# Kernel optimization log

Measured on AMD Instinct MI355X. Metric: run time of the kernel, lower is better.

Reference implementation:

```python
import jax, jax.numpy as jnp
import numpy as np

B, S, V, D, H, DK, DH, L = 1, 2048, 256, 1024, 16, 64, 4096, 4
EPS = 1e-5
SCALE = 1.0 / np.sqrt(DK)


def _ln(x, g, b):
    mu = jnp.mean(x, axis=-1, keepdims=True)
    var = jnp.mean(jnp.square(x - mu), axis=-1, keepdims=True)
    return (x - mu) * jax.lax.rsqrt(var + EPS) * g + b


def setup_inputs() -> dict:
    key = jax.random.key(0)
    ks = jax.random.split(key, 20)
    f = lambda k, shape: (0.02 * jax.random.normal(k, shape)).astype(jnp.float32)
    return {
        "x": jax.random.randint(ks[0], (B, S), 0, V),
        "emb": f(ks[1], (V, D)),
        "pos": f(ks[2], (S, D)),
        "Wq": f(ks[3], (L, D, H * DK)), "bq": jnp.zeros((L, H * DK), jnp.float32),
        "Wk": f(ks[4], (L, D, H * DK)), "bk": jnp.zeros((L, H * DK), jnp.float32),
        "Wv": f(ks[5], (L, D, H * DK)), "bv": jnp.zeros((L, H * DK), jnp.float32),
        "Wo": f(ks[6], (L, H * DK, D)),
        "ln1_g": jnp.ones((L, D), jnp.float32), "ln1_b": jnp.zeros((L, D), jnp.float32),
        "W1": f(ks[7], (L, D, DH)), "b1": jnp.zeros((L, DH), jnp.float32),
        "W2": f(ks[8], (L, DH, D)), "b2": jnp.zeros((L, D), jnp.float32),
        "ln2_g": jnp.ones((L, D), jnp.float32), "ln2_b": jnp.zeros((L, D), jnp.float32),
        "head_w": f(ks[9], (D, V)), "head_b": jnp.zeros((V,), jnp.float32),
    }


def _forward(x, emb, pos, Wq, bq, Wk, bk, Wv, bv, Wo, ln1_g, ln1_b,
             W1, b1, W2, b2, ln2_g, ln2_b, head_w, head_b):
    h = emb[x] + pos[:S]                      # [B,S,D]
    causal = jnp.tril(jnp.ones((S, S), bool))  # additive -inf above diag
    for i in range(L):
        # --- naive attention: explicit QK^T, mask, softmax, @V ---
        q = (h @ Wq[i] + bq[i]).reshape(B, S, H, DK)
        k = (h @ Wk[i] + bk[i]).reshape(B, S, H, DK)
        v = (h @ Wv[i] + bv[i]).reshape(B, S, H, DK)
        scores = jnp.einsum('bqhd,bkhd->bhqk', q * SCALE, k)   # [B,H,S,S]
        scores = jnp.where(causal[None, None], scores, -jnp.inf)
        p = jax.nn.softmax(scores, axis=-1)
        a = jnp.einsum('bhqk,bkhd->bqhd', p, v).reshape(B, S, H * DK) @ Wo[i]
        # --- TransformerLayer: x + ln2(mlp(x + ln1(attn(x)))) ---
        u = h + _ln(a, ln1_g[i], ln1_b[i])
        m = jax.nn.gelu(u @ W1[i] + b1[i], approximate=False) @ W2[i] + b2[i]
        h = h + _ln(m, ln2_g[i], ln2_b[i])
    return h @ head_w + head_b                 # [B,S,V]


def reference(x, emb, pos, Wq, bq, Wk, bk, Wv, bv, Wo, ln1_g, ln1_b,
              W1, b1, W2, b2, ln2_g, ln2_b, head_w, head_b):
    return _forward(x, emb, pos, Wq, bq, Wk, bk, Wv, bv, Wo, ln1_g, ln1_b,
                    W1, b1, W2, b2, ln2_g, ln2_b, head_w, head_b)
```

## Files before the change

kernel.cpp:

```cpp
#include <hip/hip_runtime.h>
#include <hip/hip_bf16.h>
#include <cstdint>
#include <math.h>

static constexpr int S_  = 2048;
static constexpr int D_  = 1024;
static constexpr int H_  = 16;
static constexpr int DK_ = 64;
static constexpr int DH_ = 4096;
static constexpr int L_  = 4;
static constexpr int V_  = 256;
#define ATT_SCALE 0.125f

typedef __bf16 bf16;
typedef __bf16 bf16x8 __attribute__((ext_vector_type(8)));
typedef __bf16 bf16x4v __attribute__((ext_vector_type(4)));
typedef float  f32x4  __attribute__((ext_vector_type(4)));

__device__ __forceinline__ __attribute__((address_space(3))) void* to_lds(const void* p) {
  return (__attribute__((address_space(3))) void*)(uintptr_t)p;
}
__device__ __forceinline__ __attribute__((address_space(1))) void* to_glb(const void* p) {
  return (__attribute__((address_space(1))) void*)(uintptr_t)p;
}

template <int GELU_EPI>
__global__ __launch_bounds__(256) void gemm_bf16_kernel(
    const bf16* __restrict__ A, const bf16* __restrict__ Bt,
    const float* __restrict__ bias, float* __restrict__ Cf, bf16* __restrict__ Cb,
    int M, int N, int K)
{
  __shared__ __align__(16) bf16 sA[2][128 * 64];
  __shared__ __align__(16) bf16 sB[2][64 * 64];
  const int tid  = threadIdx.x;
  const int wave = tid >> 6;
  const int lane = tid & 63;
  const int l16  = lane & 15;
  const int quad = lane >> 4;
  const int bm = blockIdx.x * 128;
  const int bn = blockIdx.y * 64;
  const int wm = (wave & 1) * 64;
  const int wn = (wave >> 1) * 32;

  const int srow = tid >> 3;
  const int sc8  = (tid & 7) ^ (srow & 7);
  const bf16* gA = A  + (size_t)(bm + srow) * K + sc8 * 8;
  const bf16* gB = Bt + (size_t)(bn + srow) * K + sc8 * 8;

  const int swz = l16 & 7;

  f32x4 acc[4][2] = {};

#pragma unroll
  for (int u = 0; u < 4; ++u)
    __builtin_amdgcn_global_load_lds(to_glb(gA + (size_t)u * 32 * K),
                                     to_lds(&sA[0][u * 2048 + tid * 8]), 16, 0, 0);
#pragma unroll
  for (int u = 0; u < 2; ++u)
    __builtin_amdgcn_global_load_lds(to_glb(gB + (size_t)u * 32 * K),
                                     to_lds(&sB[0][u * 2048 + tid * 8]), 16, 0, 0);

  int cur = 0;
  for (int k0 = 0; k0 < K; k0 += 64, cur ^= 1) {
    if (k0 + 64 < K) {
      const int nb = cur ^ 1;
      const size_t ko = k0 + 64;
#pragma unroll
      for (int u = 0; u < 4; ++u)
        __builtin_amdgcn_global_load_lds(to_glb(gA + ko + (size_t)u * 32 * K),
                                         to_lds(&sA[nb][u * 2048 + tid * 8]), 16, 0, 0);
#pragma unroll
      for (int u = 0; u < 2; ++u)
        __builtin_amdgcn_global_load_lds(to_glb(gB + ko + (size_t)u * 32 * K),
                                         to_lds(&sB[nb][u * 2048 + tid * 8]), 16, 0, 0);
      asm volatile("s_waitcnt vmcnt(6)" ::: "memory");
    } else {
      asm volatile("s_waitcnt vmcnt(0)" ::: "memory");
    }
    __builtin_amdgcn_s_barrier();

    bf16x8 af[2][4], bfv[2][2];
#pragma unroll
    for (int kc = 0; kc < 2; ++kc) {
      const int c8 = ((kc * 4 + quad) ^ swz) * 8;
#pragma unroll
      for (int i = 0; i < 4; ++i)
        af[kc][i] = *(const bf16x8*)&sA[cur][(wm + i * 16 + l16) * 64 + c8];
#pragma unroll
      for (int j = 0; j < 2; ++j)
        bfv[kc][j] = *(const bf16x8*)&sB[cur][(wn + j * 16 + l16) * 64 + c8];
    }
    asm volatile("s_waitcnt lgkmcnt(0)" ::: "memory");
    __builtin_amdgcn_s_barrier();

#pragma unroll
    for (int kc = 0; kc < 2; ++kc)
#pragma unroll
      for (int i = 0; i < 4; ++i)
#pragma unroll
        for (int j = 0; j < 2; ++j)
          acc[i][j] = __builtin_amdgcn_mfma_f32_16x16x32_bf16(af[kc][i], bfv[kc][j], acc[i][j], 0, 0, 0);
  }

#pragma unroll
  for (int i = 0; i < 4; ++i) {
#pragma unroll
    for (int j = 0; j < 2; ++j) {
      const int col = bn + wn + j * 16 + l16;
      const float bz = bias ? bias[col] : 0.0f;
#pragma unroll
      for (int r = 0; r < 4; ++r) {
        const int row = bm + wm + i * 16 + quad * 4 + r;
        float v = acc[i][j][r] + bz;
        if (GELU_EPI) v = 0.5f * v * (1.0f + erff(v * 0.70710678118654752f));
        if (Cf) Cf[(size_t)row * N + col] = v;
        if (Cb) Cb[(size_t)row * N + col] = (bf16)v;
      }
    }
  }
}

__global__ __launch_bounds__(256) void transpose_cast_kernel(
    const float* __restrict__ in, bf16* __restrict__ out, int K, int N)
{
  __shared__ float t[32][33];
  const int k0 = blockIdx.y * 32;
  const int n0 = blockIdx.x * 32;
  const int tx = threadIdx.x & 31;
  const int ty = threadIdx.x >> 5;
#pragma unroll
  for (int i = 0; i < 32; i += 8)
    t[ty + i][tx] = in[(size_t)(k0 + ty + i) * N + (n0 + tx)];
  __syncthreads();
#pragma unroll
  for (int i = 0; i < 32; i += 8)
    out[(size_t)(n0 + ty + i) * K + (k0 + tx)] = (bf16)t[tx][ty + i];
}

__global__ __launch_bounds__(256) void transpose3_cast_kernel(
    const float* __restrict__ in0, const float* __restrict__ in1, const float* __restrict__ in2,
    bf16* __restrict__ out, int K, int N)
{
  const float* in = (blockIdx.z == 0) ? in0 : (blockIdx.z == 1) ? in1 : in2;
  bf16* o = out + (size_t)blockIdx.z * K * N;
  __shared__ float t[32][33];
  const int k0 = blockIdx.y * 32;
  const int n0 = blockIdx.x * 32;
  const int tx = threadIdx.x & 31;
  const int ty = threadIdx.x >> 5;
#pragma unroll
  for (int i = 0; i < 32; i += 8)
    t[ty + i][tx] = in[(size_t)(k0 + ty + i) * N + (n0 + tx)];
  __syncthreads();
#pragma unroll
  for (int i = 0; i < 32; i += 8)
    o[(size_t)(n0 + ty + i) * K + (k0 + tx)] = (bf16)t[tx][ty + i];
}

__global__ __launch_bounds__(256) void vtrans_kernel(
    const bf16* __restrict__ qkv, bf16* __restrict__ vT)
{
  __shared__ bf16 t[32][65];
  const int s0 = blockIdx.x * 32;
  const int head = blockIdx.y;
  const int sr = threadIdx.x >> 3, d8 = (threadIdx.x & 7) * 8;
  bf16x8 v = *(const bf16x8*)(qkv + (size_t)(s0 + sr) * (3 * D_) + 2 * D_ + head * DK_ + d8);
#pragma unroll
  for (int i = 0; i < 8; ++i) t[sr][d8 + i] = v[i];
  __syncthreads();
  const int dw = threadIdx.x >> 2, s4 = (threadIdx.x & 3) * 8;
  bf16x8 o;
#pragma unroll
  for (int i = 0; i < 8; ++i) o[i] = t[s4 + i][dw];
  *(bf16x8*)(vT + (size_t)head * DK_ * S_ + (size_t)dw * S_ + s0 + s4) = o;
}

__global__ __launch_bounds__(256) void embed_kernel(
    const int* __restrict__ x, const float* __restrict__ emb, const float* __restrict__ pos,
    float* __restrict__ hf, bf16* __restrict__ hb)
{
  const int s = blockIdx.x;
  const int d = threadIdx.x * 4;
  const int tok = x[s];
  const float4 e = *(const float4*)(emb + (size_t)tok * D_ + d);
  const float4 p = *(const float4*)(pos + (size_t)s * D_ + d);
  float4 o; o.x = e.x + p.x; o.y = e.y + p.y; o.z = e.z + p.z; o.w = e.w + p.w;
  *(float4*)(hf + (size_t)s * D_ + d) = o;
  bf16x4v ob = {(bf16)o.x, (bf16)o.y, (bf16)o.z, (bf16)o.w};
  *(bf16x4v*)(hb + (size_t)s * D_ + d) = ob;
}

__device__ __forceinline__ float wave_reduce_sum(float v) {
#pragma unroll
  for (int off = 32; off > 0; off >>= 1) v += __shfl_xor(v, off, 64);
  return v;
}

__global__ __launch_bounds__(256) void ln_add_kernel(
    const float* __restrict__ src, const float* __restrict__ resid,
    const float* __restrict__ g, const float* __restrict__ b,
    float* __restrict__ outf, bf16* __restrict__ outb)
{
  const int r = blockIdx.x;
  const int t = threadIdx.x;
  const float4 x = ((const float4*)(src + (size_t)r * D_))[t];
  float s  = x.x + x.y + x.z + x.w;
  float s2 = x.x * x.x + x.y * x.y + x.z * x.z + x.w * x.w;
  s  = wave_reduce_sum(s);
  s2 = wave_reduce_sum(s2);
  __shared__ float red[8];
  const int wave = t >> 6, lane = t & 63;
  if (lane == 0) { red[wave] = s; red[4 + wave] = s2; }
  __syncthreads();
  s  = red[0] + red[1] + red[2] + red[3];
  s2 = red[4] + red[5] + red[6] + red[7];
  const float mu  = s * (1.0f / 1024.0f);
  const float var = s2 * (1.0f / 1024.0f) - mu * mu;
  const float rs  = rsqrtf(var + 1e-5f);
  const float4 gv = ((const float4*)g)[t];
  const float4 bv = ((const float4*)b)[t];
  const float4 hv = ((const float4*)(resid + (size_t)r * D_))[t];
  const float o0 = hv.x + (x.x - mu) * rs * gv.x + bv.x;
  const float o1 = hv.y + (x.y - mu) * rs * gv.y + bv.y;
  const float o2 = hv.z + (x.z - mu) * rs * gv.z + bv.z;
  const float o3 = hv.w + (x.w - mu) * rs * gv.w + bv.w;
  if (outf) { float4 o4; o4.x = o0; o4.y = o1; o4.z = o2; o4.w = o3;
              ((float4*)(outf + (size_t)r * D_))[t] = o4; }
  if (outb) { bf16x4v ob = {(bf16)o0, (bf16)o1, (bf16)o2, (bf16)o3};
              ((bf16x4v*)(outb + (size_t)r * D_))[t] = ob; }
}

__global__ __launch_bounds__(256) void attn_mfma_kernel(
    const bf16* __restrict__ qkv, const bf16* __restrict__ vT, bf16* __restrict__ out)
{
  __shared__ __align__(16) bf16 sK[64 * 64];
  __shared__ __align__(16) bf16 sV[64 * 64];
  __shared__ __align__(16) bf16 sP[4][16 * 64];

  const int head = blockIdx.y;
  const int xb   = blockIdx.x;
  const int qIdx = (head & 8) ? (31 - xb) : xb;
  const int qb   = qIdx * 64;
  const int tid  = threadIdx.x;
  const int wave = tid >> 6, lane = tid & 63;
  const int l16  = lane & 15, quad = lane >> 4;
  const int swz  = l16 & 7;

  const size_t rstr = 3 * D_;
  const bf16* kbase = qkv + D_ + head * DK_;
  const bf16* vbase = vT + (size_t)head * DK_ * S_;

  const int srow   = tid >> 3;
  const int kchunk = (tid & 7) ^ (srow & 7);

  bf16x8 aq0, aq1;
  {
    const bf16* qrow = qkv + (size_t)(qb + wave * 16 + l16) * rstr + head * DK_ + quad * 8;
    aq0 = *(const bf16x8*)(qrow);
    aq1 = *(const bf16x8*)(qrow + 32);
  }

  f32x4 oa[4] = {};
  float lsum[4] = {0.0f, 0.0f, 0.0f, 0.0f};
  const int qrow0 = qb + wave * 16 + quad * 4;

  for (int j0 = 0; j0 <= qb + 63; j0 += 64) {
    __syncthreads();
#pragma unroll
    for (int u = 0; u < 2; ++u) {
      const int r = u * 32 + srow;
      __builtin_amdgcn_global_load_lds(to_glb(kbase + (size_t)(j0 + r) * rstr + kchunk * 8),
                                       to_lds(sK + u * 2048 + tid * 8), 16, 0, 0);
      __builtin_amdgcn_global_load_lds(to_glb(vbase + (size_t)r * S_ + j0 + kchunk * 8),
                                       to_lds(sV + u * 2048 + tid * 8), 16, 0, 0);
    }
    __syncthreads();

    f32x4 sc[4];
#pragma unroll
    for (int n = 0; n < 4; ++n) {
      const bf16* kr = &sK[(n * 16 + l16) * 64];
      bf16x8 bk0 = *(const bf16x8*)(kr + ((quad    ) ^ swz) * 8);
      bf16x8 bk1 = *(const bf16x8*)(kr + ((quad + 4) ^ swz) * 8);
      f32x4 z = {};
      z = __builtin_amdgcn_mfma_f32_16x16x32_bf16(aq0, bk0, z, 0, 0, 0);
      z = __builtin_amdgcn_mfma_f32_16x16x32_bf16(aq1, bk1, z, 0, 0, 0);
      sc[n] = z;
    }
    bf16 pb[4][4];
#pragma unroll
    for (int n = 0; n < 4; ++n) {
      const int key = j0 + n * 16 + l16;
#pragma unroll
      for (int r = 0; r < 4; ++r) {
        const float p = (key <= qrow0 + r) ? __expf(sc[n][r] * ATT_SCALE) : 0.0f;
        lsum[r] += p;
        pb[n][r] = (bf16)p;
      }
    }
    bf16* pw = &sP[wave][0];
    const int cb = l16 >> 3, co = l16 & 7;
#pragma unroll
    for (int n = 0; n < 4; ++n) {
#pragma unroll
      for (int r = 0; r < 4; ++r) {
        const int row = quad * 4 + r;
        const int ch = (2 * n + cb) ^ (row & 7);
        pw[row * 64 + ch * 8 + co] = pb[n][r];
      }
    }
    __asm__ volatile("s_waitcnt lgkmcnt(0)" ::: "memory");
    __builtin_amdgcn_wave_barrier();
    bf16x8 ap0 = *(const bf16x8*)&pw[l16 * 64 + ((quad    ) ^ swz) * 8];
    bf16x8 ap1 = *(const bf16x8*)&pw[l16 * 64 + ((quad + 4) ^ swz) * 8];

#pragma unroll
    for (int n = 0; n < 4; ++n) {
      const bf16* vr = &sV[(n * 16 + l16) * 64];
      bf16x8 bv0 = *(const bf16x8*)(vr + ((quad    ) ^ swz) * 8);
      bf16x8 bv1 = *(const bf16x8*)(vr + ((quad + 4) ^ swz) * 8);
      oa[n] = __builtin_amdgcn_mfma_f32_16x16x32_bf16(ap0, bv0, oa[n], 0, 0, 0);
      oa[n] = __builtin_amdgcn_mfma_f32_16x16x32_bf16(ap1, bv1, oa[n], 0, 0, 0);
    }
  }

#pragma unroll
  for (int r = 0; r < 4; ++r) {
#pragma unroll
    for (int off = 1; off <= 8; off <<= 1)
      lsum[r] += __shfl_xor(lsum[r], off, 64);
  }
#pragma unroll
  for (int r = 0; r < 4; ++r) {
    const float inv = 1.0f / lsum[r];
    const int qrow = qrow0 + r;
#pragma unroll
    for (int n = 0; n < 4; ++n)
      out[(size_t)qrow * D_ + head * DK_ + n * 16 + l16] = (bf16)(oa[n][r] * inv);
  }
}

__global__ __launch_bounds__(256) void pack3_kernel(
    const float* __restrict__ a, const float* __restrict__ b, const float* __restrict__ c,
    float* __restrict__ out)
{
  const int i = blockIdx.x * 256 + threadIdx.x;
  if (i < 1024) out[i] = a[i];
  else if (i < 2048) out[i] = b[i - 1024];
  else if (i < 3072) out[i] = c[i - 2048];
}

extern "C" void kernel_launch(void* const* d_in, const int* in_sizes, int n_in,
                              void* d_out, int out_size, void* d_ws, size_t ws_size,
                              hipStream_t stream)
{
  const int*   x     = (const int*)d_in[0];
  const float* emb   = (const float*)d_in[1];
  const float* pos   = (const float*)d_in[2];
  const float* Wq    = (const float*)d_in[3];
  const float* bq    = (const float*)d_in[4];
  const float* Wk    = (const float*)d_in[5];
  const float* bk    = (const float*)d_in[6];
  const float* Wv    = (const float*)d_in[7];
  const float* bv    = (const float*)d_in[8];
  const float* Wo    = (const float*)d_in[9];
  const float* ln1g  = (const float*)d_in[10];
  const float* ln1b  = (const float*)d_in[11];
  const float* W1    = (const float*)d_in[12];
  const float* b1    = (const float*)d_in[13];
  const float* W2    = (const float*)d_in[14];
  const float* b2    = (const float*)d_in[15];
  const float* ln2g  = (const float*)d_in[16];
  const float* ln2b  = (const float*)d_in[17];
  const float* headw = (const float*)d_in[18];
  const float* headb = (const float*)d_in[19];

  char* w = (char*)d_ws;
  float* h_f32   = (float*)w;  w += (size_t)S_ * D_ * 4;
  bf16*  h_b     = (bf16*)w;   w += (size_t)S_ * D_ * 2;
  bf16*  qkv_b   = (bf16*)w;   w += (size_t)S_ * 3 * D_ * 2;
  bf16*  attn_b  = (bf16*)w;   w += (size_t)S_ * D_ * 2;
  float* a_f32   = (float*)w;  w += (size_t)S_ * D_ * 4;
  bf16*  u_b     = (bf16*)w;   w += (size_t)S_ * D_ * 2;
  bf16*  mh_b    = (bf16*)w;   w += (size_t)S_ * DH_ * 2;
  float* m_f32   = (float*)w;  w += (size_t)S_ * D_ * 4;
  bf16*  qkvT    = (bf16*)w;   w += (size_t)3 * D_ * D_ * 2;
  bf16*  woT     = (bf16*)w;   w += (size_t)D_ * D_ * 2;
  bf16*  w1T     = (bf16*)w;   w += (size_t)DH_ * D_ * 2;
  bf16*  w2T     = (bf16*)w;   w += (size_t)D_ * DH_ * 2;
  bf16*  headT   = (bf16*)w;   w += (size_t)V_ * D_ * 2;
  float* qkvbias = (float*)w;  w += (size_t)3 * D_ * 4;
  bf16*  vT      = qkvT;

  embed_kernel<<<dim3(S_), dim3(256), 0, stream>>>(x, emb, pos, h_f32, h_b);
  transpose_cast_kernel<<<dim3(V_ / 32, D_ / 32), dim3(256), 0, stream>>>(headw, headT, D_, V_);

  for (int i = 0; i < L_; ++i) {
    const float* Wq_i = Wq + (size_t)i * D_ * D_;
    const float* Wk_i = Wk + (size_t)i * D_ * D_;
    const float* Wv_i = Wv + (size_t)i * D_ * D_;
    const float* Wo_i = Wo + (size_t)i * D_ * D_;
    const float* W1_i = W1 + (size_t)i * D_ * DH_;
    const float* W2_i = W2 + (size_t)i * DH_ * D_;

    transpose3_cast_kernel<<<dim3(D_ / 32, D_ / 32, 3), dim3(256), 0, stream>>>(
        Wq_i, Wk_i, Wv_i, qkvT, D_, D_);
    pack3_kernel<<<dim3(12), dim3(256), 0, stream>>>(bq + (size_t)i * D_, bk + (size_t)i * D_, bv + (size_t)i * D_, qkvbias);
    gemm_bf16_kernel<0><<<dim3(S_ / 128, 3 * D_ / 64), dim3(256), 0, stream>>>(
        h_b, qkvT, qkvbias, nullptr, qkv_b, S_, 3 * D_, D_);
    vtrans_kernel<<<dim3(S_ / 32, H_), dim3(256), 0, stream>>>(qkv_b, vT);
    attn_mfma_kernel<<<dim3(S_ / 64, H_), dim3(256), 0, stream>>>(qkv_b, vT, attn_b);
    transpose_cast_kernel<<<dim3(D_ / 32, D_ / 32), dim3(256), 0, stream>>>(Wo_i, woT, D_, D_);
    gemm_bf16_kernel<0><<<dim3(S_ / 128, D_ / 64), dim3(256), 0, stream>>>(
        attn_b, woT, nullptr, a_f32, nullptr, S_, D_, D_);
    ln_add_kernel<<<dim3(S_), dim3(256), 0, stream>>>(
        a_f32, h_f32, ln1g + (size_t)i * D_, ln1b + (size_t)i * D_, nullptr, u_b);
    transpose_cast_kernel<<<dim3(DH_ / 32, D_ / 32), dim3(256), 0, stream>>>(W1_i, w1T, D_, DH_);
    gemm_bf16_kernel<1><<<dim3(S_ / 128, DH_ / 64), dim3(256), 0, stream>>>(
        u_b, w1T, b1 + (size_t)i * DH_, nullptr, mh_b, S_, DH_, D_);
    transpose_cast_kernel<<<dim3(D_ / 32, DH_ / 32), dim3(256), 0, stream>>>(W2_i, w2T, DH_, D_);
    gemm_bf16_kernel<0><<<dim3(S_ / 128, D_ / 64), dim3(256), 0, stream>>>(
        mh_b, w2T, b2 + (size_t)i * D_, m_f32, nullptr, S_, D_, DH_);
    ln_add_kernel<<<dim3(S_), dim3(256), 0, stream>>>(
        m_f32, h_f32, ln2g + (size_t)i * D_, ln2b + (size_t)i * D_, h_f32, h_b);
  }

  gemm_bf16_kernel<0><<<dim3(S_ / 128, V_ / 64), dim3(256), 0, stream>>>(
      h_b, headT, headb, (float*)d_out, nullptr, S_, V_, D_);
}
```

Before: 907.7 us.

## Double-buffer K/V tiles in attention kernel and pre-scale Q

Attention kernel now double-buffers K and V tiles in LDS, prefetching the next 64-key tile via global_load_lds while computing on the current one, using vmcnt waits and raw s_barriers. The softmax scale is folded into Q once at load time instead of multiplying every score. This aims to hide global-load latency behind MFMA work, at the cost of doubled LDS use (lower occupancy) and hand-managed wait counts. Pre-scaling Q in bf16 adds slight rounding differences.

```diff
diff --git a/kernel.cpp b/kernel.cpp
--- a/kernel.cpp
+++ b/kernel.cpp
@@ -233,8 +233,8 @@
 __global__ __launch_bounds__(256) void attn_mfma_kernel(
     const bf16* __restrict__ qkv, const bf16* __restrict__ vT, bf16* __restrict__ out)
 {
-  __shared__ __align__(16) bf16 sK[64 * 64];
-  __shared__ __align__(16) bf16 sV[64 * 64];
+  __shared__ __align__(16) bf16 sK[2][64 * 64];
+  __shared__ __align__(16) bf16 sV[2][64 * 64];
   __shared__ __align__(16) bf16 sP[4][16 * 64];
 
   const int head = blockIdx.y;
@@ -256,30 +256,52 @@
   bf16x8 aq0, aq1;
   {
     const bf16* qrow = qkv + (size_t)(qb + wave * 16 + l16) * rstr + head * DK_ + quad * 8;
-    aq0 = *(const bf16x8*)(qrow);
-    aq1 = *(const bf16x8*)(qrow + 32);
+    bf16x8 t0 = *(const bf16x8*)(qrow);
+    bf16x8 t1 = *(const bf16x8*)(qrow + 32);
+#pragma unroll
+    for (int i = 0; i < 8; ++i) {
+      aq0[i] = (bf16)((float)t0[i] * ATT_SCALE);
+      aq1[i] = (bf16)((float)t1[i] * ATT_SCALE);
+    }
   }
 
   f32x4 oa[4] = {};
   float lsum[4] = {0.0f, 0.0f, 0.0f, 0.0f};
   const int qrow0 = qb + wave * 16 + quad * 4;
-
-  for (int j0 = 0; j0 <= qb + 63; j0 += 64) {
-    __syncthreads();
-#pragma unroll
-    for (int u = 0; u < 2; ++u) {
-      const int r = u * 32 + srow;
-      __builtin_amdgcn_global_load_lds(to_glb(kbase + (size_t)(j0 + r) * rstr + kchunk * 8),
-                                       to_lds(sK + u * 2048 + tid * 8), 16, 0, 0);
-      __builtin_amdgcn_global_load_lds(to_glb(vbase + (size_t)r * S_ + j0 + kchunk * 8),
-                                       to_lds(sV + u * 2048 + tid * 8), 16, 0, 0);
-    }
-    __syncthreads();
+  const int jmax = qb + 63;
+
+#pragma unroll
+  for (int u = 0; u < 2; ++u) {
+    const int r = u * 32 + srow;
+    __builtin_amdgcn_global_load_lds(to_glb(kbase + (size_t)r * rstr + kchunk * 8),
+                                     to_lds(&sK[0][u * 2048 + tid * 8]), 16, 0, 0);
+    __builtin_amdgcn_global_load_lds(to_glb(vbase + (size_t)r * S_ + kchunk * 8),
+                                     to_lds(&sV[0][u * 2048 + tid * 8]), 16, 0, 0);
+  }
+
+  int cur = 0;
+  for (int j0 = 0; j0 <= jmax; j0 += 64, cur ^= 1) {
+    if (j0 + 64 <= jmax) {
+      const int nb = cur ^ 1;
+      const int jn = j0 + 64;
+#pragma unroll
+      for (int u = 0; u < 2; ++u) {
+        const int r = u * 32 + srow;
+        __builtin_amdgcn_global_load_lds(to_glb(kbase + (size_t)(jn + r) * rstr + kchunk * 8),
+                                         to_lds(&sK[nb][u * 2048 + tid * 8]), 16, 0, 0);
+        __builtin_amdgcn_global_load_lds(to_glb(vbase + (size_t)r * S_ + jn + kchunk * 8),
+                                         to_lds(&sV[nb][u * 2048 + tid * 8]), 16, 0, 0);
+      }
+      asm volatile("s_waitcnt vmcnt(4)" ::: "memory");
+    } else {
+      asm volatile("s_waitcnt vmcnt(0)" ::: "memory");
+    }
+    __builtin_amdgcn_s_barrier();
 
     f32x4 sc[4];
 #pragma unroll
     for (int n = 0; n < 4; ++n) {
-      const bf16* kr = &sK[(n * 16 + l16) * 64];
+      const bf16* kr = &sK[cur][(n * 16 + l16) * 64];
       bf16x8 bk0 = *(const bf16x8*)(kr + ((quad    ) ^ swz) * 8);
       bf16x8 bk1 = *(const bf16x8*)(kr + ((quad + 4) ^ swz) * 8);
       f32x4 z = {};
@@ -293,7 +315,7 @@
       const int key = j0 + n * 16 + l16;
 #pragma unroll
       for (int r = 0; r < 4; ++r) {
-        const float p = (key <= qrow0 + r) ? __expf(sc[n][r] * ATT_SCALE) : 0.0f;
+        const float p = (key <= qrow0 + r) ? __expf(sc[n][r]) : 0.0f;
         lsum[r] += p;
         pb[n][r] = (bf16)p;
       }
@@ -309,19 +331,21 @@
         pw[row * 64 + ch * 8 + co] = pb[n][r];
       }
     }
-    __asm__ volatile("s_waitcnt lgkmcnt(0)" ::: "memory");
+    asm volatile("s_waitcnt lgkmcnt(0)" ::: "memory");
     __builtin_amdgcn_wave_barrier();
     bf16x8 ap0 = *(const bf16x8*)&pw[l16 * 64 + ((quad    ) ^ swz) * 8];
     bf16x8 ap1 = *(const bf16x8*)&pw[l16 * 64 + ((quad + 4) ^ swz) * 8];
 
 #pragma unroll
     for (int n = 0; n < 4; ++n) {
-      const bf16* vr = &sV[(n * 16 + l16) * 64];
+      const bf16* vr = &sV[cur][(n * 16 + l16) * 64];
       bf16x8 bv0 = *(const bf16x8*)(vr + ((quad    ) ^ swz) * 8);
       bf16x8 bv1 = *(const bf16x8*)(vr + ((quad + 4) ^ swz) * 8);
       oa[n] = __builtin_amdgcn_mfma_f32_16x16x32_bf16(ap0, bv0, oa[n], 0, 0, 0);
       oa[n] = __builtin_amdgcn_mfma_f32_16x16x32_bf16(ap1, bv1, oa[n], 0, 0, 0);
     }
+    asm volatile("s_waitcnt lgkmcnt(0)" ::: "memory");
+    __builtin_amdgcn_s_barrier();
   }
 
 #pragma unroll
```

After: 875.5 us. 1.04x faster.
